# Optimization experiments

Hardware: AMD Instinct MI355X
Metric: run time of the kernel (lower is better)

Reference implementation:

```python
import jax, jax.numpy as jnp
import numpy as np

H, NH, NKV, D, I, T, B = 4096, 32, 8, 128, 12288, 1024, 128
THETA, EPS = 1e6, 1e-6


def setup_inputs() -> dict:
    ks = iter(jax.random.split(jax.random.key(0), 64))

    def randn(s):
        return jax.random.normal(next(ks), s, jnp.float32)

    def qw(o, i):
        return jax.random.randint(next(ks), (o, i), 0, 16, jnp.int32)

    def sc(o, g):
        return jax.random.uniform(next(ks), (o, g), jnp.float32, 0.005, 0.02)

    def rot(g):  # block-diagonal rotation, one 128x128 block per input group
        return randn((g, B, B)) / np.float32(np.sqrt(B))

    return dict(
        positions=jnp.arange(T, dtype=jnp.int32),
        hidden_states=randn((T, H)),
        residual=randn((T, H)),
        w_in=jnp.ones(H, jnp.float32), w_post=jnp.ones(H, jnp.float32),
        w_qn=jnp.ones(D, jnp.float32), w_kn=jnp.ones(D, jnp.float32),
        R_q=rot(H // B), qw_q=qw(NH * D, H), sc_q=sc(NH * D, H // B),
        R_k=rot(H // B), qw_k=qw(NKV * D, H), sc_k=sc(NKV * D, H // B),
        R_v=rot(H // B), qw_v=qw(NKV * D, H), sc_v=sc(NKV * D, H // B),
        R_o=rot(NH * D // B), qw_o=qw(H, NH * D), sc_o=sc(H, NH * D // B),
        R_g=rot(H // B), qw_g=qw(I, H), sc_g=sc(I, H // B),
        R_u=rot(H // B), qw_u=qw(I, H), sc_u=sc(I, H // B),
        R_d=rot(I // B), qw_d=qw(H, I), sc_d=sc(H, I // B),
    )


def _rmsnorm(x, w):
    return x * jax.lax.rsqrt(jnp.mean(x * x, -1, keepdims=True) + EPS) * w


def _rot_lin(x, R, qw, sc):
    # RotateLinearInt4: block-rotate input, then int4 group-dequant GEMM.
    G = R.shape[0]
    xr = jnp.einsum('tgi,gij->tgj', x.reshape(-1, G, B), R).reshape(x.shape)
    O = qw.shape[0]
    W = ((qw.astype(x.dtype) - 8.0).reshape(O, G, B) * sc[:, :, None]).reshape(O, G * B)
    return xr @ W.T


def _rope(pos, x):  # neox-style rope, x: [T, h, D]
    half = D // 2
    inv = jnp.power(jnp.float32(THETA), -(jnp.arange(half, dtype=jnp.float32) * (2.0 / D)))
    f = pos.astype(jnp.float32)[:, None] * inv  # [T, half]
    cos, sin = jnp.cos(f)[:, None, :], jnp.sin(f)[:, None, :]
    x1, x2 = x[..., :half], x[..., half:]
    return jnp.concatenate([x1 * cos - x2 * sin, x2 * cos + x1 * sin], -1)


def _forward(positions, hidden_states, residual, w_in, w_post, w_qn, w_kn,
             R_q, qw_q, sc_q, R_k, qw_k, sc_k, R_v, qw_v, sc_v,
             R_o, qw_o, sc_o, R_g, qw_g, sc_g, R_u, qw_u, sc_u,
             R_d, qw_d, sc_d):
    res = hidden_states + residual            # fused add+RMSNorm path
    x = _rmsnorm(res, w_in)
    q = _rot_lin(x, R_q, qw_q, sc_q).reshape(T, NH, D)
    k = _rot_lin(x, R_k, qw_k, sc_k).reshape(T, NKV, D)
    v = _rot_lin(x, R_v, qw_v, sc_v).reshape(T, NKV, D)
    q = _rmsnorm(q, w_qn)                     # per-head q/k RMSNorm
    k = _rmsnorm(k, w_kn)
    q = _rope(positions, q)
    k = _rope(positions, k)
    rep = NH // NKV                           # GQA: repeat kv heads
    kk = jnp.repeat(k, rep, axis=1)
    vv = jnp.repeat(v, rep, axis=1)
    scores = jnp.einsum('thd,shd->hts', q, kk) * (D ** -0.5)
    mask = jnp.tril(jnp.ones((T, T), bool))
    scores = jnp.where(mask, scores, jnp.finfo(scores.dtype).min)
    probs = jax.nn.softmax(scores, -1)
    attn = jnp.einsum('hts,shd->thd', probs, vv).reshape(T, NH * D)
    h = _rot_lin(attn, R_o, qw_o, sc_o)
    res2 = h + res
    x2 = _rmsnorm(res2, w_post)
    gate = _rot_lin(x2, R_g, qw_g, sc_g)
    up = _rot_lin(x2, R_u, qw_u, sc_u)
    h2 = _rot_lin(jax.nn.silu(gate) * up, R_d, qw_d, sc_d)
    return h2, res2


def reference(positions, hidden_states, residual, w_in, w_post, w_qn, w_kn,
              R_q, qw_q, sc_q, R_k, qw_k, sc_k, R_v, qw_v, sc_v,
              R_o, qw_o, sc_o, R_g, qw_g, sc_g, R_u, qw_u, sc_u,
              R_d, qw_d, sc_d):
    return _forward(positions, hidden_states, residual, w_in, w_post, w_qn, w_kn,
                    R_q, qw_q, sc_q, R_k, qw_k, sc_k, R_v, qw_v, sc_v,
                    R_o, qw_o, sc_o, R_g, qw_g, sc_g, R_u, qw_u, sc_u,
                    R_d, qw_d, sc_d)
```

## Files before the change

### kernel.cpp

```cpp
#include <hip/hip_runtime.h>

typedef unsigned short u16;
typedef __attribute__((ext_vector_type(4))) float   f32x4;
typedef __attribute__((ext_vector_type(8))) __bf16  bf16x8;
typedef __attribute__((ext_vector_type(4))) __bf16  bf16x4;
typedef __attribute__((ext_vector_type(8))) short   short8;
typedef __attribute__((ext_vector_type(4))) int     int32x4;
typedef __attribute__((ext_vector_type(4))) short   short4v;

#define MFMA16(a,b,c) __builtin_amdgcn_mfma_f32_16x16x32_bf16(a,b,c,0,0,0)

static __device__ __forceinline__ u16 f2bf(float f){
  unsigned u = __builtin_bit_cast(unsigned, f);
  return (u16)((u + 0x7fffu + ((u >> 16) & 1u)) >> 16);
}
static __device__ __forceinline__ float bf2f(u16 h){
  return __builtin_bit_cast(float, ((unsigned)h) << 16);
}
static __device__ __forceinline__ bf16x8 ldb16(const u16* p){
  return __builtin_bit_cast(bf16x8, *(const short8*)p);
}
static __device__ __forceinline__ void gload_lds16(const void* g, void* l){
  __builtin_amdgcn_global_load_lds(
      reinterpret_cast<const __attribute__((address_space(1))) unsigned int*>(
          reinterpret_cast<unsigned long long>(g)),
      reinterpret_cast<__attribute__((address_space(3))) unsigned int*>(
          reinterpret_cast<unsigned long long>(l)),
      16, 0, 0);
}

static constexpr int T_ = 1024, H_ = 4096, NH_ = 32, NKV_ = 8, I_ = 12288;

__global__ __launch_bounds__(256) void addnorm_kernel(
    const float* __restrict__ a, const float* __restrict__ b,
    const float* __restrict__ w, float* __restrict__ res_out,
    u16* __restrict__ x_out)
{
  const int t = blockIdx.x, tid = threadIdx.x;
  __shared__ float red[4];
  float vals[16]; float ss = 0.f;
  const size_t base = (size_t)t * H_;
  #pragma unroll
  for (int i = 0; i < 16; ++i){
    int c = tid + i*256;
    float v = a[base + c];
    if (b) v += b[base + c];
    vals[i] = v; ss += v*v;
  }
  #pragma unroll
  for (int off = 32; off; off >>= 1) ss += __shfl_xor(ss, off);
  if ((tid & 63) == 0) red[tid >> 6] = ss;
  __syncthreads();
  float tot = red[0] + red[1] + red[2] + red[3];
  float rn = rsqrtf(tot / (float)H_ + 1e-6f);
  #pragma unroll
  for (int i = 0; i < 16; ++i){
    int c = tid + i*256;
    if (res_out) res_out[base + c] = vals[i];
    x_out[base + c] = f2bf(vals[i] * rn * w[c]);
  }
}

__global__ __launch_bounds__(256) void rprep_kernel(
    const float* __restrict__ Rq, const float* __restrict__ Rk,
    const float* __restrict__ Rv, const float* __restrict__ Ro,
    const float* __restrict__ Rg_, const float* __restrict__ Ru,
    const float* __restrict__ Rd, u16* __restrict__ Rt)
{
  __shared__ float sR[128][129];
  const int b = blockIdx.x, tid = threadIdx.x;
  const float* src;
  if      (b <  32) src = Rq  + (size_t)(b      ) * 16384;
  else if (b <  64) src = Rk  + (size_t)(b -  32) * 16384;
  else if (b <  96) src = Rv  + (size_t)(b -  64) * 16384;
  else if (b < 128) src = Ro  + (size_t)(b -  96) * 16384;
  else if (b < 160) src = Rg_ + (size_t)(b - 128) * 16384;
  else if (b < 192) src = Ru  + (size_t)(b - 160) * 16384;
  else              src = Rd  + (size_t)(b - 192) * 16384;
  #pragma unroll
  for (int it = 0; it < 16; ++it){
    int idx = (it*256 + tid) * 4;
    float4 v = *(const float4*)&src[idx];
    int i = idx >> 7, j = idx & 127;
    sR[i][j] = v.x; sR[i][j+1] = v.y; sR[i][j+2] = v.z; sR[i][j+3] = v.w;
  }
  __syncthreads();
  u16* dst = Rt + (size_t)b * 16384;
  #pragma unroll
  for (int it = 0; it < 32; ++it){
    int idx = it*256 + tid;
    int j = idx >> 6, i2 = (idx & 63) * 2;
    unsigned lo = f2bf(sR[i2][j]), hi = f2bf(sR[i2+1][j]);
    *(unsigned*)&dst[j*128 + i2] = lo | (hi << 16);
  }
}

__global__ __launch_bounds__(256) void rot_kernel(
    const u16* __restrict__ X, const u16* __restrict__ Rt,
    u16* __restrict__ Y, int LD)
{
  __shared__ u16 sX[64][136];
  __shared__ u16 sRt[128][136];
  const int g = blockIdx.y, m0 = blockIdx.x * 64, tid = threadIdx.x;
  #pragma unroll
  for (int i = 0; i < 4; ++i){
    int vid = i*256 + tid, r = vid >> 4, c = (vid & 15) * 8;
    *(short8*)&sX[r][c] = *(const short8*)&X[(size_t)(m0 + r) * LD + g*128 + c];
  }
  const u16* Rg = Rt + (size_t)g * 16384;
  #pragma unroll
  for (int it = 0; it < 8; ++it){
    int idx = it*256 + tid;
    int j = idx >> 4, c8 = (idx & 15) * 8;
    *(short8*)&sRt[j][c8] = *(const short8*)&Rg[j*128 + c8];
  }
  __syncthreads();
  const int lane = tid & 63, w = tid >> 6;
  const int fr = lane & 15, fq = lane >> 4, nw = w * 32;
  f32x4 acc[4][2];
  #pragma unroll
  for (int mi=0;mi<4;mi++)
    #pragma unroll
    for (int ni=0;ni<2;ni++) acc[mi][ni] = (f32x4){0.f,0.f,0.f,0.f};
  #pragma unroll
  for (int kk = 0; kk < 128; kk += 32){
    bf16x8 af[4], bv[2];
    #pragma unroll
    for (int mi=0;mi<4;mi++) af[mi] = ldb16(&sX[mi*16 + fr][kk + fq*8]);
    #pragma unroll
    for (int ni=0;ni<2;ni++) bv[ni] = ldb16(&sRt[nw + ni*16 + fr][kk + fq*8]);
    #pragma unroll
    for (int mi=0;mi<4;mi++)
      #pragma unroll
      for (int ni=0;ni<2;ni++)
        acc[mi][ni] = MFMA16(af[mi], bv[ni], acc[mi][ni]);
  }
  #pragma unroll
  for (int mi=0;mi<4;mi++)
    #pragma unroll
    for (int ni=0;ni<2;ni++)
      #pragma unroll
      for (int rg=0;rg<4;rg++){
        int m = m0 + mi*16 + fq*4 + rg;
        int n = g*128 + nw + ni*16 + fr;
        Y[(size_t)m * LD + n] = f2bf(acc[mi][ni][rg]);
      }
}

template<int NF, bool PARTIAL, bool OUT_BF16>
__global__ __launch_bounds__(512, 1) void gemm_deq(
    const u16* __restrict__ A, const int* __restrict__ QW,
    const float* __restrict__ SC, void* __restrict__ Cout,
    int N, int K, int kc, int nN)
{
  __shared__ u16 sA[2][16384];
  __shared__ u16 sB[2][NF * 4096];
  const int tid = threadIdx.x;
  const int lane = tid & 63, w = tid >> 6;
  const int nblk = gridDim.x, q8 = nblk >> 3, b = blockIdx.x;
  const int l = (b & 7) * q8 + (b >> 3);
  const int mt = l & 3, rest = l >> 2;
  const int nt = rest % nN, z = rest / nN;
  const int bm0 = mt * 256, bn0 = nt * (NF * 64);
  const int kbase = z * kc;
  const int KG = K >> 7;
  const int nkt = kc >> 6;

  f32x4 acc[8][NF];
  #pragma unroll
  for (int i=0;i<8;i++)
    #pragma unroll
    for (int j=0;j<NF;j++) acc[i][j] = (f32x4){0.f,0.f,0.f,0.f};

  const int wr = (w >> 2) * 128, wc = (w & 3) * (NF * 16);
  const int fr = lane & 15, fq = lane >> 4;

  const int l8 = lane >> 3;
  const size_t K2 = (size_t)K * 2;
  const char* gA0 = (const char*)A
      + ((size_t)(bm0 + w*32 + l8) * K + (size_t)kbase) * 2
      + (((lane & 7) * 16) ^ (l8 << 4));
  auto ADMA = [&](int kt, int c){
    const char* g = gA0 + (size_t)kt * 128;
    char* lb = (char*)&sA[c][0] + (w*32) * 128;
    #pragma unroll
    for (int i=0;i<4;i++)
      gload_lds16(g + (size_t)(i*8) * K2, lb + i*1024);
  };

  const int rBr = tid >> 4, cB4 = (tid & 15) * 4;
  const int* gB0 = QW + (size_t)(bn0 + rBr) * K + kbase + cB4;
  const float* gS0 = SC + (size_t)(bn0 + rBr) * KG;
  const int sBx = (cB4 * 2) ^ ((rBr & 7) << 4);

  int32x4 rB[2*NF];
  float   rS[2*NF];
  auto loadB = [&](int kt){
    const int* gb = gB0 + kt*64;
    const int g = (kbase + kt*64) >> 7;
    const float* ps = gS0 + g;
    #pragma unroll
    for (int i=0;i<2*NF;i++){
      rB[i] = *(const int32x4*)(gb + (size_t)i*32*K);
      rS[i] = ps[(size_t)i*32*KG];
    }
  };
  auto storeB = [&](int c){
    #pragma unroll
    for (int i=0;i<2*NF;i++){
      float s = rS[i], ns = -8.f * s;
      bf16x4 o;
      o[0] = (__bf16)fmaf((float)rB[i].x, s, ns);
      o[1] = (__bf16)fmaf((float)rB[i].y, s, ns);
      o[2] = (__bf16)fmaf((float)rB[i].z, s, ns);
      o[3] = (__bf16)fmaf((float)rB[i].w, s, ns);
      *(bf16x4*)((char*)&sB[c][0] + (rBr + 32*i)*128 + sBx) = o;
    }
  };

  auto mfma_half = [&](int c, int kk){
    bf16x8 af[8], bv[NF];
    #pragma unroll
    for (int mi=0;mi<8;mi++){
      int r = wr + mi*16 + fr;
      af[mi] = *(const bf16x8*)((const char*)&sA[c][0] + r*128 +
                ((kk*64 + fq*16) ^ ((r & 7) << 4)));
    }
    #pragma unroll
    for (int ni=0;ni<NF;ni++){
      int r = wc + ni*16 + fr;
      bv[ni] = *(const bf16x8*)((const char*)&sB[c][0] + r*128 +
                ((kk*64 + fq*16) ^ ((r & 7) << 4)));
    }
    __builtin_amdgcn_s_setprio(1);
    #pragma unroll
    for (int mi=0;mi<8;mi++)
      #pragma unroll
      for (int ni=0;ni<NF;ni++)
        acc[mi][ni] = MFMA16(af[mi], bv[ni], acc[mi][ni]);
    __builtin_amdgcn_s_setprio(0);
  };

  loadB(0);
  ADMA(0, 0);
  asm volatile("s_waitcnt vmcnt(4)" ::: "memory");
  __builtin_amdgcn_sched_barrier(0);
  storeB(0);
  asm volatile("s_waitcnt vmcnt(0) lgkmcnt(0)" ::: "memory");
  __builtin_amdgcn_s_barrier();

  int cb = 0;
  for (int t = 0; t < nkt; ++t){
    const bool more = (t + 1) < nkt;
    if (more){
      loadB(t+1);
      ADMA(t+1, cb ^ 1);
      __builtin_amdgcn_sched_barrier(0);
    }
    mfma_half(cb, 0);
    mfma_half(cb, 1);
    if (more){
      asm volatile("s_waitcnt vmcnt(4)" ::: "memory");
      __builtin_amdgcn_sched_barrier(0);
      storeB(cb ^ 1);
      asm volatile("s_waitcnt vmcnt(0) lgkmcnt(0)" ::: "memory");
      __builtin_amdgcn_sched_barrier(0);
      __builtin_amdgcn_s_barrier();
      cb ^= 1;
    }
  }

  #pragma unroll
  for (int mi=0;mi<8;mi++)
    #pragma unroll
    for (int ni=0;ni<NF;ni++)
      #pragma unroll
      for (int rg=0;rg<4;rg++){
        size_t m = bm0 + wr + mi*16 + fq*4 + rg;
        size_t n = bn0 + wc + ni*16 + fr;
        float v = acc[mi][ni][rg];
        if (PARTIAL)          ((float*)Cout)[((size_t)z*1024 + m) * N + n] = v;
        else if (OUT_BF16)    ((u16*)Cout)[m * N + n] = f2bf(v);
        else                  ((float*)Cout)[m * N + n] = v;
      }
}

__global__ __launch_bounds__(256) void reduce_splits(
    const float* __restrict__ P, int nsplit, int n,
    const float* __restrict__ addend, float* __restrict__ outf, u16* __restrict__ outb)
{
  size_t base = ((size_t)blockIdx.x*256 + threadIdx.x) * 4;
  if (base >= (size_t)n) return;
  f32x4 s = *(const f32x4*)&P[base];
  for (int j = 1; j < nsplit; ++j)
    s += *(const f32x4*)&P[(size_t)j*n + base];
  if (addend) s += *(const f32x4*)&addend[base];
  if (outb){
    short4v o;
    #pragma unroll
    for (int e=0;e<4;e++) o[e] = (short)f2bf(s[e]);
    *(short4v*)&outb[base] = o;
  } else {
    *(f32x4*)&outf[base] = s;
  }
}

__global__ __launch_bounds__(64) void qknorm_rope_kernel(
    const float* __restrict__ in, const float* __restrict__ w,
    const int* __restrict__ pos, u16* __restrict__ out, int nh)
{
  const int t = blockIdx.x, h = blockIdx.y, j = threadIdx.x;
  const float* row = in + ((size_t)t * nh + h) * 128;
  float x1 = row[j], x2 = row[j + 64];
  float ss = x1*x1 + x2*x2;
  #pragma unroll
  for (int off = 32; off; off >>= 1) ss += __shfl_xor(ss, off);
  float rn = rsqrtf(ss / 128.f + 1e-6f);
  float xn1 = x1 * rn * w[j], xn2 = x2 * rn * w[j + 64];
  float inv = exp2f(-(float)j * (19.93156856932417f / 64.f));
  float f = (float)pos[t] * inv;
  float sv, cv; sincosf(f, &sv, &cv);
  u16* orow = out + ((size_t)t * nh + h) * 128;
  orow[j]      = f2bf(xn1 * cv - xn2 * sv);
  orow[j + 64] = f2bf(xn2 * cv + xn1 * sv);
}

__global__ __launch_bounds__(256) void attn_kernel(
    const u16* __restrict__ Q, const u16* __restrict__ Kc,
    const u16* __restrict__ Vc, u16* __restrict__ O)
{
  __shared__ u16 sK[32][128];
  __shared__ u16 sVt[128][32];
  __shared__ u16 sP[4][16][32];
  const int qt = blockIdx.x, h = blockIdx.y, kvh = h >> 2;
  const int tid = threadIdx.x, lane = tid & 63, w = tid >> 6;
  const int fr = lane & 15, fq = lane >> 4;
  const int r0 = qt*64 + w*16;
  const float scale = 0.08838834764831845f;
  bf16x8 aq[4];
  #pragma unroll
  for (int kd=0;kd<4;kd++)
    aq[kd] = ldb16(&Q[(size_t)(r0 + fr) * 4096 + h*128 + kd*32 + fq*8]);
  f32x4 accO[8];
  #pragma unroll
  for (int ni=0;ni<8;ni++) accO[ni] = (f32x4){0.f,0.f,0.f,0.f};
  float mrow[4] = {-1e30f,-1e30f,-1e30f,-1e30f};
  float lrow[4] = {0.f,0.f,0.f,0.f};
  const int ntiles = (qt + 1) * 2;
  for (int jt = 0; jt < ntiles; ++jt){
    __syncthreads();
    #pragma unroll
    for (int i=0;i<2;i++){
      int vid = i*256 + tid, r = vid >> 4, c = (vid & 15) * 8;
      *(short8*)&sK[r][c] = *(const short8*)&Kc[(size_t)(jt*32 + r) * 1024 + kvh*128 + c];
      short8 vv = *(const short8*)&Vc[(size_t)(jt*32 + r) * 1024 + kvh*128 + c];
      const u16* pv = (const u16*)&vv;
      #pragma unroll
      for (int e=0;e<8;e++) sVt[c + e][r] = pv[e];
    }
    __syncthreads();
    f32x4 accS[2]; accS[0] = (f32x4){0.f,0.f,0.f,0.f}; accS[1] = accS[0];
    #pragma unroll
    for (int kd=0;kd<4;kd++){
      #pragma unroll
      for (int ni=0;ni<2;ni++){
        bf16x8 bk = ldb16(&sK[ni*16 + fr][kd*32 + fq*8]);
        accS[ni] = MFMA16(aq[kd], bk, accS[ni]);
      }
    }
    float s[2][4];
    #pragma unroll
    for (int ni=0;ni<2;ni++)
      #pragma unroll
      for (int rg=0;rg<4;rg++){
        int row = r0 + fq*4 + rg, col = jt*32 + ni*16 + fr;
        float v = accS[ni][rg] * scale;
        s[ni][rg] = (col <= row) ? v : -1e30f;
      }
    float alpha[4];
    #pragma unroll
    for (int rg=0;rg<4;rg++){
      float mx = fmaxf(s[0][rg], s[1][rg]);
      #pragma unroll
      for (int off=1; off<16; off<<=1) mx = fmaxf(mx, __shfl_xor(mx, off, 16));
      float mnew = fmaxf(mrow[rg], mx);
      alpha[rg] = __expf(mrow[rg] - mnew);
      mrow[rg] = mnew;
      float p0 = __expf(s[0][rg] - mnew), p1 = __expf(s[1][rg] - mnew);
      s[0][rg] = p0; s[1][rg] = p1;
      float ps = p0 + p1;
      #pragma unroll
      for (int off=1; off<16; off<<=1) ps += __shfl_xor(ps, off, 16);
      lrow[rg] = lrow[rg] * alpha[rg] + ps;
    }
    #pragma unroll
    for (int ni=0;ni<2;ni++)
      #pragma unroll
      for (int rg=0;rg<4;rg++)
        sP[w][fq*4 + rg][ni*16 + fr] = f2bf(s[ni][rg]);
    __syncthreads();
    #pragma unroll
    for (int ni=0;ni<8;ni++)
      #pragma unroll
      for (int rg=0;rg<4;rg++) accO[ni][rg] *= alpha[rg];
    bf16x8 ap = ldb16(&sP[w][fr][fq*8]);
    #pragma unroll
    for (int ni=0;ni<8;ni++){
      bf16x8 bv = ldb16(&sVt[ni*16 + fr][fq*8]);
      accO[ni] = MFMA16(ap, bv, accO[ni]);
    }
  }
  #pragma unroll
  for (int ni=0;ni<8;ni++)
    #pragma unroll
    for (int rg=0;rg<4;rg++){
      int row = r0 + fq*4 + rg, col = h*128 + ni*16 + fr;
      O[(size_t)row * 4096 + col] = f2bf(accO[ni][rg] / lrow[rg]);
    }
}

__global__ __launch_bounds__(256) void silu_mul_kernel(
    const u16* __restrict__ g, const u16* __restrict__ u, u16* __restrict__ o, int n)
{
  int i = blockIdx.x * 256 + threadIdx.x;
  if (i < n){
    float gv = bf2f(g[i]), uv = bf2f(u[i]);
    o[i] = f2bf(gv / (1.f + __expf(-gv)) * uv);
  }
}

extern "C" void kernel_launch(void* const* d_in, const int* in_sizes, int n_in,
                              void* d_out, int out_size, void* d_ws, size_t ws_size,
                              hipStream_t stream)
{
  const int*   positions = (const int*)  d_in[0];
  const float* hs    = (const float*)d_in[1];
  const float* resid = (const float*)d_in[2];
  const float* w_in  = (const float*)d_in[3];
  const float* w_post= (const float*)d_in[4];
  const float* w_qn  = (const float*)d_in[5];
  const float* w_kn  = (const float*)d_in[6];
  const float* R_q = (const float*)d_in[7];
  const int*   qw_q= (const int*)  d_in[8];
  const float* sc_q= (const float*)d_in[9];
  const float* R_k = (const float*)d_in[10];
  const int*   qw_k= (const int*)  d_in[11];
  const float* sc_k= (const float*)d_in[12];
  const float* R_v = (const float*)d_in[13];
  const int*   qw_v= (const int*)  d_in[14];
  const float* sc_v= (const float*)d_in[15];
  const float* R_o = (const float*)d_in[16];
  const int*   qw_o= (const int*)  d_in[17];
  const float* sc_o= (const float*)d_in[18];
  const float* R_g = (const float*)d_in[19];
  const int*   qw_g= (const int*)  d_in[20];
  const float* sc_g= (const float*)d_in[21];
  const float* R_u = (const float*)d_in[22];
  const int*   qw_u= (const int*)  d_in[23];
  const float* sc_u= (const float*)d_in[24];
  const float* R_d = (const float*)d_in[25];
  const int*   qw_d= (const int*)  d_in[26];
  const float* sc_d= (const float*)d_in[27];
  (void)in_sizes; (void)n_in; (void)out_size; (void)ws_size;

  char* wsp = (char*)d_ws; size_t off = 0;
  auto alloc = [&](size_t bytes)->void*{
    void* p = wsp + off; off += (bytes + 255) & ~(size_t)255; return p;
  };
  float* res  = (float*)alloc((size_t)T_*H_*4);
  u16*   xbf  = (u16*)  alloc((size_t)T_*H_*2);
  u16*   xrA  = (u16*)  alloc((size_t)T_*H_*2);
  u16*   xrB  = (u16*)  alloc((size_t)T_*H_*2);
  u16*   xrC  = (u16*)  alloc((size_t)T_*H_*2);
  float* qf   = (float*)alloc((size_t)T_*4096*4);
  float* kf   = (float*)alloc((size_t)T_*1024*4);
  u16*   qbf  = (u16*)  alloc((size_t)T_*4096*2);
  u16*   kbf  = (u16*)  alloc((size_t)T_*1024*2);
  u16*   vbf  = (u16*)  alloc((size_t)T_*1024*2);
  u16*   abf  = (u16*)  alloc((size_t)T_*4096*2);
  u16*   gbf  = (u16*)  alloc((size_t)T_*I_*2);
  u16*   ubf  = (u16*)  alloc((size_t)T_*I_*2);
  u16*   hbf  = (u16*)  alloc((size_t)T_*I_*2);
  u16*   Rtb  = (u16*)  alloc((size_t)288*16384*2);
  u16*   hrbf = gbf;

  float* pQKV = (float*)gbf;
  float* pO   = (float*)gbf;
  float* pD   = (float*)wsp;

  float* h2   = (float*)d_out;
  float* res2 = (float*)d_out + (size_t)T_*H_;

  rprep_kernel<<<288, 256, 0, stream>>>(R_q, R_k, R_v, R_o, R_g, R_u, R_d, Rtb);
  addnorm_kernel<<<T_, 256, 0, stream>>>(hs, resid, w_in, res, xbf);
  rot_kernel<<<dim3(16,32),256,0,stream>>>(xbf, Rtb +   (size_t)0*16384, xrA, H_);
  rot_kernel<<<dim3(16,32),256,0,stream>>>(xbf, Rtb +  (size_t)32*16384, xrB, H_);
  rot_kernel<<<dim3(16,32),256,0,stream>>>(xbf, Rtb +  (size_t)64*16384, xrC, H_);
  gemm_deq<4,true ,false><<<256,512,0,stream>>>(xrA, qw_q, sc_q, pQKV, 4096, 4096, 1024, 16);
  reduce_splits<<<(T_*4096)/1024,256,0,stream>>>(pQKV, 4, T_*4096, nullptr, qf, nullptr);
  gemm_deq<4,true ,false><<<128,512,0,stream>>>(xrB, qw_k, sc_k, pQKV, 1024, 4096, 512, 4);
  reduce_splits<<<(T_*1024)/1024,256,0,stream>>>(pQKV, 8, T_*1024, nullptr, kf, nullptr);
  gemm_deq<4,true ,false><<<128,512,0,stream>>>(xrC, qw_v, sc_v, pQKV, 1024, 4096, 512, 4);
  reduce_splits<<<(T_*1024)/1024,256,0,stream>>>(pQKV, 8, T_*1024, nullptr, nullptr, vbf);
  qknorm_rope_kernel<<<dim3(T_,NH_ ),64,0,stream>>>(qf, w_qn, positions, qbf, NH_);
  qknorm_rope_kernel<<<dim3(T_,NKV_),64,0,stream>>>(kf, w_kn, positions, kbf, NKV_);
  attn_kernel<<<dim3(16,32),256,0,stream>>>(qbf, kbf, vbf, abf);
  rot_kernel<<<dim3(16,32),256,0,stream>>>(abf, Rtb + (size_t)96*16384, xrA, H_);
  gemm_deq<4,true ,false><<<256,512,0,stream>>>(xrA, qw_o, sc_o, pO, 4096, 4096, 1024, 16);
  reduce_splits<<<(T_*4096)/1024,256,0,stream>>>(pO, 4, T_*4096, res, res2, nullptr);
  addnorm_kernel<<<T_,256,0,stream>>>(res2, nullptr, w_post, nullptr, xbf);
  rot_kernel<<<dim3(16,32),256,0,stream>>>(xbf, Rtb + (size_t)128*16384, xrA, H_);
  rot_kernel<<<dim3(16,32),256,0,stream>>>(xbf, Rtb + (size_t)160*16384, xrB, H_);
  gemm_deq<3,false,true ><<<256,512,0,stream>>>(xrA, qw_g, sc_g, gbf, 12288, 4096, 4096, 64);
  gemm_deq<3,false,true ><<<256,512,0,stream>>>(xrB, qw_u, sc_u, ubf, 12288, 4096, 4096, 64);
  silu_mul_kernel<<<(T_*I_)/256,256,0,stream>>>(gbf, ubf, hbf, T_*I_);
  rot_kernel<<<dim3(16,96),256,0,stream>>>(hbf, Rtb + (size_t)192*16384, hrbf, I_);
  gemm_deq<4,true ,false><<<256,512,0,stream>>>(hrbf, qw_d, sc_d, pD, 4096, 12288, 3072, 16);
  reduce_splits<<<(T_*4096)/1024,256,0,stream>>>(pD, 4, T_*4096, nullptr, h2, nullptr);
}
```

Before: 912.9 us.

## Batch rotation launches, fuse SiLU-mul into up GEMM, pad attention LDS, resplit K/V

The Q/K/V rotations and the gate/up rotations each become one launch, with blockIdx.y choosing the rotation block and the output buffer. SiLU(gate)*up is computed in the up GEMM epilogue by reading the stored gate tensor, which removes the separate elementwise kernel and its extra pass over a large intermediate. The K and V GEMMs now use 256 blocks with a split-K of 16 instead of 128 blocks with a split of 8, which fills more CUs but doubles the partial-sum traffic. Attention shared-memory arrays are padded to cut bank conflicts.

```diff
diff --git a/kernel.cpp b/kernel.cpp
--- a/kernel.cpp
+++ b/kernel.cpp
@@ -97,17 +97,20 @@
 
 __global__ __launch_bounds__(256) void rot_kernel(
     const u16* __restrict__ X, const u16* __restrict__ Rt,
-    u16* __restrict__ Y, int LD)
+    u16* __restrict__ Y0, u16* __restrict__ Y1, u16* __restrict__ Y2,
+    int LD, int gpt)
 {
   __shared__ u16 sX[64][136];
   __shared__ u16 sRt[128][136];
-  const int g = blockIdx.y, m0 = blockIdx.x * 64, tid = threadIdx.x;
+  const int by = blockIdx.y, g = by % gpt;
+  const int m0 = blockIdx.x * 64, tid = threadIdx.x;
+  u16* Y = (by < gpt) ? Y0 : (by < 2*gpt ? Y1 : Y2);
   #pragma unroll
   for (int i = 0; i < 4; ++i){
     int vid = i*256 + tid, r = vid >> 4, c = (vid & 15) * 8;
     *(short8*)&sX[r][c] = *(const short8*)&X[(size_t)(m0 + r) * LD + g*128 + c];
   }
-  const u16* Rg = Rt + (size_t)g * 16384;
+  const u16* Rg = Rt + (size_t)by * 16384;
   #pragma unroll
   for (int it = 0; it < 8; ++it){
     int idx = it*256 + tid;
@@ -151,7 +154,7 @@
 __global__ __launch_bounds__(512, 1) void gemm_deq(
     const u16* __restrict__ A, const int* __restrict__ QW,
     const float* __restrict__ SC, void* __restrict__ Cout,
-    int N, int K, int kc, int nN)
+    int N, int K, int kc, int nN, const u16* __restrict__ gate)
 {
   __shared__ u16 sA[2][16384];
   __shared__ u16 sB[2][NF * 4096];
@@ -280,7 +283,13 @@
         size_t n = bn0 + wc + ni*16 + fr;
         float v = acc[mi][ni][rg];
         if (PARTIAL)          ((float*)Cout)[((size_t)z*1024 + m) * N + n] = v;
-        else if (OUT_BF16)    ((u16*)Cout)[m * N + n] = f2bf(v);
+        else if (OUT_BF16){
+          if (gate){
+            float gv = bf2f(gate[m * N + n]);
+            v *= gv / (1.f + __expf(-gv));
+          }
+          ((u16*)Cout)[m * N + n] = f2bf(v);
+        }
         else                  ((float*)Cout)[m * N + n] = v;
       }
 }
@@ -329,9 +338,9 @@
     const u16* __restrict__ Q, const u16* __restrict__ Kc,
     const u16* __restrict__ Vc, u16* __restrict__ O)
 {
-  __shared__ u16 sK[32][128];
-  __shared__ u16 sVt[128][32];
-  __shared__ u16 sP[4][16][32];
+  __shared__ u16 sK[32][136];
+  __shared__ u16 sVt[128][40];
+  __shared__ u16 sP[4][16][40];
   const int qt = blockIdx.x, h = blockIdx.y, kvh = h >> 2;
   const int tid = threadIdx.x, lane = tid & 63, w = tid >> 6;
   const int fr = lane & 15, fq = lane >> 4;
@@ -417,16 +426,6 @@
       int row = r0 + fq*4 + rg, col = h*128 + ni*16 + fr;
       O[(size_t)row * 4096 + col] = f2bf(accO[ni][rg] / lrow[rg]);
     }
-}
-
-__global__ __launch_bounds__(256) void silu_mul_kernel(
-    const u16* __restrict__ g, const u16* __restrict__ u, u16* __restrict__ o, int n)
-{
-  int i = blockIdx.x * 256 + threadIdx.x;
-  if (i < n){
-    float gv = bf2f(g[i]), uv = bf2f(u[i]);
-    o[i] = f2bf(gv / (1.f + __expf(-gv)) * uv);
-  }
 }
 
 extern "C" void kernel_launch(void* const* d_in, const int* in_sizes, int n_in,
@@ -493,28 +492,24 @@
 
   rprep_kernel<<<288, 256, 0, stream>>>(R_q, R_k, R_v, R_o, R_g, R_u, R_d, Rtb);
   addnorm_kernel<<<T_, 256, 0, stream>>>(hs, resid, w_in, res, xbf);
-  rot_kernel<<<dim3(16,32),256,0,stream>>>(xbf, Rtb +   (size_t)0*16384, xrA, H_);
-  rot_kernel<<<dim3(16,32),256,0,stream>>>(xbf, Rtb +  (size_t)32*16384, xrB, H_);
-  rot_kernel<<<dim3(16,32),256,0,stream>>>(xbf, Rtb +  (size_t)64*16384, xrC, H_);
-  gemm_deq<4,true ,false><<<256,512,0,stream>>>(xrA, qw_q, sc_q, pQKV, 4096, 4096, 1024, 16);
+  rot_kernel<<<dim3(16,96),256,0,stream>>>(xbf, Rtb, xrA, xrB, xrC, H_, 32);
+  gemm_deq<4,true ,false><<<256,512,0,stream>>>(xrA, qw_q, sc_q, pQKV, 4096, 4096, 1024, 16, nullptr);
   reduce_splits<<<(T_*4096)/1024,256,0,stream>>>(pQKV, 4, T_*4096, nullptr, qf, nullptr);
-  gemm_deq<4,true ,false><<<128,512,0,stream>>>(xrB, qw_k, sc_k, pQKV, 1024, 4096, 512, 4);
-  reduce_splits<<<(T_*1024)/1024,256,0,stream>>>(pQKV, 8, T_*1024, nullptr, kf, nullptr);
-  gemm_deq<4,true ,false><<<128,512,0,stream>>>(xrC, qw_v, sc_v, pQKV, 1024, 4096, 512, 4);
-  reduce_splits<<<(T_*1024)/1024,256,0,stream>>>(pQKV, 8, T_*1024, nullptr, nullptr, vbf);
+  gemm_deq<4,true ,false><<<256,512,0,stream>>>(xrB, qw_k, sc_k, pQKV, 1024, 4096, 256, 4, nullptr);
+  reduce_splits<<<(T_*1024)/1024,256,0,stream>>>(pQKV, 16, T_*1024, nullptr, kf, nullptr);
+  gemm_deq<4,true ,false><<<256,512,0,stream>>>(xrC, qw_v, sc_v, pQKV, 1024, 4096, 256, 4, nullptr);
+  reduce_splits<<<(T_*1024)/1024,256,0,stream>>>(pQKV, 16, T_*1024, nullptr, nullptr, vbf);
   qknorm_rope_kernel<<<dim3(T_,NH_ ),64,0,stream>>>(qf, w_qn, positions, qbf, NH_);
   qknorm_rope_kernel<<<dim3(T_,NKV_),64,0,stream>>>(kf, w_kn, positions, kbf, NKV_);
   attn_kernel<<<dim3(16,32),256,0,stream>>>(qbf, kbf, vbf, abf);
-  rot_kernel<<<dim3(16,32),256,0,stream>>>(abf, Rtb + (size_t)96*16384, xrA, H_);
-  gemm_deq<4,true ,false><<<256,512,0,stream>>>(xrA, qw_o, sc_o, pO, 4096, 4096, 1024, 16);
+  rot_kernel<<<dim3(16,32),256,0,stream>>>(abf, Rtb + (size_t)96*16384, xrA, nullptr, nullptr, H_, 32);
+  gemm_deq<4,true ,false><<<256,512,0,stream>>>(xrA, qw_o, sc_o, pO, 4096, 4096, 1024, 16, nullptr);
   reduce_splits<<<(T_*4096)/1024,256,0,stream>>>(pO, 4, T_*4096, res, res2, nullptr);
   addnorm_kernel<<<T_,256,0,stream>>>(res2, nullptr, w_post, nullptr, xbf);
-  rot_kernel<<<dim3(16,32),256,0,stream>>>(xbf, Rtb + (size_t)128*16384, xrA, H_);
-  rot_kernel<<<dim3(16,32),256,0,stream>>>(xbf, Rtb + (size_t)160*16384, xrB, H_);
-  gemm_deq<3,false,true ><<<256,512,0,stream>>>(xrA, qw_g, sc_g, gbf, 12288, 4096, 4096, 64);
-  gemm_deq<3,false,true ><<<256,512,0,stream>>>(xrB, qw_u, sc_u, ubf, 12288, 4096, 4096, 64);
-  silu_mul_kernel<<<(T_*I_)/256,256,0,stream>>>(gbf, ubf, hbf, T_*I_);
-  rot_kernel<<<dim3(16,96),256,0,stream>>>(hbf, Rtb + (size_t)192*16384, hrbf, I_);
-  gemm_deq<4,true ,false><<<256,512,0,stream>>>(hrbf, qw_d, sc_d, pD, 4096, 12288, 3072, 16);
+  rot_kernel<<<dim3(16,64),256,0,stream>>>(xbf, Rtb + (size_t)128*16384, xrA, xrB, nullptr, H_, 32);
+  gemm_deq<3,false,true ><<<256,512,0,stream>>>(xrA, qw_g, sc_g, gbf, 12288, 4096, 4096, 64, nullptr);
+  gemm_deq<3,false,true ><<<256,512,0,stream>>>(xrB, qw_u, sc_u, hbf, 12288, 4096, 4096, 64, gbf);
+  rot_kernel<<<dim3(16,96),256,0,stream>>>(hbf, Rtb + (size_t)192*16384, hrbf, nullptr, nullptr, I_, 96);
+  gemm_deq<4,true ,false><<<256,512,0,stream>>>(hrbf, qw_d, sc_d, pD, 4096, 12288, 3072, 16, nullptr);
   reduce_splits<<<(T_*4096)/1024,256,0,stream>>>(pD, 4, T_*4096, nullptr, h2, nullptr);
 }
```

Result: no change. 898.6 us (-1.6%).
